# Performance work log

Measured on AMD Instinct MI355X. Metric: run time of the kernel, lower is better.

Reference implementation:

```python
import jax, jax.numpy as jnp
import numpy as np

N_USERS = 10000
N_ITEMS = 40000
HID = 64
NNZ = 2_000_000
B = 8192
N_TOT = N_USERS + N_ITEMS
HOP = 3


def setup_inputs() -> dict:
    key = jax.random.key(0)
    ks = jax.random.split(key, 13)
    emb = lambda k, n: jax.random.normal(k, (n, HID), dtype=jnp.float32) * (1.0 / np.sqrt(HID))
    # Dense social adjacency; scaled so repeated propagation stays numerically stable
    S = jax.random.uniform(ks[6], (N_USERS, N_USERS), dtype=jnp.float32) * (2.0 / N_USERS)
    return {
        "users": jax.random.randint(ks[0], (B,), 0, N_USERS),
        "pos": jax.random.randint(ks[1], (B,), 0, N_ITEMS),
        "neg": jax.random.randint(ks[2], (B,), 0, N_ITEMS),
        "user_embs": emb(ks[3], N_USERS),
        "item_embs": emb(ks[4], N_ITEMS),
        "user1_embs": emb(ks[5], N_USERS),
        "item1_embs": emb(ks[7], N_ITEMS),
        "user2_embs": emb(ks[8], N_USERS),
        "item2_embs": emb(ks[9], N_ITEMS),
        "S": S,
        "A_rows": jax.random.randint(ks[10], (NNZ,), 0, N_TOT, dtype=jnp.int32),
        "A_cols": jax.random.randint(ks[11], (NNZ,), 0, N_TOT, dtype=jnp.int32),
        "A_vals": jax.random.uniform(ks[12], (NNZ,), dtype=jnp.float32) * (1.0 / 40.0),
        "hop": HOP,
    }


def social_gcn(uemb, S, hop):
    # LightGCN-style propagation over dense social graph; mean over layers 0..hop
    h = uemb
    acc = uemb
    for _ in range(hop):
        h = S @ h                      # [n_users, hid] dense GEMM
        acc = acc + h
    return acc / (hop + 1)


def ui_gcn(uemb, iemb, rows, cols, vals, hop):
    # LightGCN over sparse bipartite user-item graph of size [N_TOT, N_TOT]
    ego = jnp.concatenate([uemb, iemb], axis=0)   # [N_TOT, hid]
    h = ego
    acc = ego
    for _ in range(hop):
        msgs = vals[:, None] * h[cols]            # gather + scale  [nnz, hid]
        h = jax.ops.segment_sum(msgs, rows, num_segments=N_TOT)
        acc = acc + h
    out = acc / (hop + 1)
    return out[:N_USERS], out[N_USERS:]


def reference(users, pos, neg, user_embs, item_embs, user1_embs, item1_embs,
              user2_embs, item2_embs, S, A_rows, A_cols, A_vals, hop):
    all_user_S = social_gcn(user_embs, S, hop)
    all_user_A, all_item = ui_gcn(user_embs, item_embs, A_rows, A_cols, A_vals, hop)
    all_user = 0.5 * all_user_S + 0.5 * all_user_A

    all_user_social = social_gcn(user1_embs, S, hop)
    all_item_social = item1_embs
    all_user_rating, all_item_rating = ui_gcn(user2_embs, item2_embs, A_rows, A_cols, A_vals, hop)

    return (all_user[users], all_item[pos], all_item[neg],
            all_user_S, all_user_A,
            all_user_social[users], all_item_social[pos], all_item_social[neg],
            all_user_rating[users], all_item_rating[pos], all_item_rating[neg])
```

## Files before the change

kernel.cpp:

```cpp
#include <hip/hip_runtime.h>

#define N_USERS 10000
#define N_ITEMS 40000
#define N_TOTAL 50000
#define HID     64
#define BATCH   8192
#define HOPS    3
#define KDIM    10000
#define KTILES  157
#define KPAD    (KTILES * 64)
#define SPLITK  4
#define NSOC    (KTILES * SPLITK)

#define O0 0
#define O1 524288
#define O2 1048576
#define O3 1572864
#define O4 2212864
#define O5 2852864
#define O6 3377152
#define O7 3901440
#define O8 4425728
#define O9 4950016
#define O10 5474304

typedef __attribute__((ext_vector_type(8))) short short8;
typedef __attribute__((ext_vector_type(4))) float floatx4;
typedef __attribute__((ext_vector_type(4))) unsigned short ushort4v;
typedef __attribute__((ext_vector_type(8))) unsigned short ushort8v;

__device__ __forceinline__ unsigned short f32bf(float f) {
  union { float f; unsigned u; } v; v.f = f;
  unsigned r = v.u + 0x7fffu + ((v.u >> 16) & 1u);
  return (unsigned short)(r >> 16);
}

__global__ __launch_bounds__(256)
void init_all(const float* __restrict__ ue, const float* __restrict__ u1,
              const float* __restrict__ ie, const float* __restrict__ u2,
              const float* __restrict__ i2, const int* __restrict__ Arows,
              int* __restrict__ counts, int nnz,
              float* __restrict__ HS0, float* __restrict__ HS1, float* __restrict__ HSacc,
              float* __restrict__ E0, float* __restrict__ Eacc) {
  int b = blockIdx.x, t = threadIdx.x;
  if (b < 2500) {
    int i = b * 256 + t;
    int r = i >> 6, c = i & 63;
    float a = ue[i], x = u1[i];
    size_t p = (size_t)r * 128 + c;
    HS0[p] = a; HS0[p + 64] = x;
    HSacc[p] = a; HSacc[p + 64] = x;
    HS1[p] = 0.f; HS1[p + 64] = 0.f;
  } else if (b < 15000) {
    int i = (b - 2500) * 256 + t;
    int r = i >> 6;
    float a, x;
    if (r < N_USERS) { a = ue[i]; x = u2[i]; }
    else             { a = ie[i - N_USERS * HID]; x = i2[i - N_USERS * HID]; }
    size_t p = (size_t)r * 128 + (i & 63);
    E0[p] = a; E0[p + 64] = x;
    Eacc[p] = a; Eacc[p + 64] = x;
  } else {
    int i = (b - 15000) * 256 + t;
    if (i < nnz) atomicAdd(&counts[Arows[i]], 1);
  }
}

__global__ void scan1(const int* __restrict__ counts, int* __restrict__ offs, int* __restrict__ bsum) {
  __shared__ int sh[256];
  int t = threadIdx.x;
  int base = blockIdx.x * 1024 + t * 4;
  int v0 = 0, v1 = 0, v2 = 0, v3 = 0;
  if (base + 0 < N_TOTAL) v0 = counts[base + 0];
  if (base + 1 < N_TOTAL) v1 = counts[base + 1];
  if (base + 2 < N_TOTAL) v2 = counts[base + 2];
  if (base + 3 < N_TOTAL) v3 = counts[base + 3];
  int s = v0 + v1 + v2 + v3;
  sh[t] = s;
  __syncthreads();
  for (int d = 1; d < 256; d <<= 1) {
    int x = (t >= d) ? sh[t - d] : 0;
    __syncthreads();
    sh[t] += x;
    __syncthreads();
  }
  int excl = sh[t] - s;
  if (t == 255) bsum[blockIdx.x] = sh[255];
  if (base + 0 < N_TOTAL) offs[base + 0] = excl; excl += v0;
  if (base + 1 < N_TOTAL) offs[base + 1] = excl; excl += v1;
  if (base + 2 < N_TOTAL) offs[base + 2] = excl; excl += v2;
  if (base + 3 < N_TOTAL) offs[base + 3] = excl;
}

__global__ void scan2(int* __restrict__ bsum, int nb) {
  __shared__ int sh[64];
  int t = threadIdx.x;
  int v = (t < nb) ? bsum[t] : 0;
  sh[t] = v;
  __syncthreads();
  for (int d = 1; d < 64; d <<= 1) {
    int x = (t >= d) ? sh[t - d] : 0;
    __syncthreads();
    sh[t] += x;
    __syncthreads();
  }
  if (t < nb) bsum[t] = sh[t] - v;
}

__device__ __forceinline__ void transpose_dev(int kb, const float* __restrict__ H,
                                              unsigned short* __restrict__ Ht,
                                              float* __restrict__ ts) {
  int k0 = kb * 64;
  int t = threadIdx.x;
#pragma unroll
  for (int i = 0; i < 8; i++) {
    int f = t + i * 256;
    int r = f >> 5, c4 = (f & 31) * 4;
    float4 v = make_float4(0.f, 0.f, 0.f, 0.f);
    if (k0 + r < KDIM) v = *(const float4*)&H[(size_t)(k0 + r) * 128 + c4];
    *(float4*)&ts[r * 132 + c4] = v;
  }
  __syncthreads();
#pragma unroll
  for (int i = 0; i < 4; i++) {
    int g = t + i * 256;
    int n = g >> 3, ko = (g & 7) * 8;
    ushort8v o;
#pragma unroll
    for (int j = 0; j < 8; j++) o[j] = f32bf(ts[(ko + j) * 132 + n]);
    *(ushort8v*)&Ht[(size_t)n * KPAD + k0 + ko] = o;
  }
}

__global__ __launch_bounds__(256)
void scan3_tr(int* __restrict__ offs, const int* __restrict__ bexcl,
              int* __restrict__ cursor, int nnz,
              const float* __restrict__ hc, unsigned short* __restrict__ Ht) {
  __shared__ __align__(16) float ts[64 * 132];
  if (blockIdx.x < 196) {
    int i = blockIdx.x * 256 + threadIdx.x;
    if (i < N_TOTAL) {
      int v = offs[i] + bexcl[i >> 10];
      offs[i] = v; cursor[i] = v;
    }
    if (i == 0) offs[N_TOTAL] = nnz;
  } else {
    transpose_dev(blockIdx.x - 196, hc, Ht, ts);
  }
}

__global__ void scatter_csr(const int* __restrict__ rows, const int* __restrict__ cols,
                            const float* __restrict__ vals, int* __restrict__ cursor,
                            int2* __restrict__ edges, int n) {
  int i = blockIdx.x * 256 + threadIdx.x;
  if (i < n) {
    int p = atomicAdd(&cursor[rows[i]], 1);
    edges[p] = make_int2(cols[i], __float_as_int(vals[i]));
  }
}

template<int H>
__global__ __launch_bounds__(256)
void social_gemm(const float* __restrict__ S, unsigned short* __restrict__ Sb,
                 const unsigned short* __restrict__ Bt, float* __restrict__ Cdst) {
  __shared__ __align__(16) unsigned short As[64 * 72];
  __shared__ __align__(16) unsigned short Bs[128 * 72];
  int tid = threadIdx.x;
  int mt = blockIdx.x % KTILES;
  int ks = blockIdx.x / KTILES;
  int m0 = mt * 64;
  int t0 = (ks * KTILES) / SPLITK;
  int t1 = ((ks + 1) * KTILES) / SPLITK;
  int wave = tid >> 6, lane = tid & 63;
  int mq = lane & 15, quad = lane >> 4;

  floatx4 acc[8];
#pragma unroll
  for (int i = 0; i < 8; i++) acc[i] = (floatx4){0.f, 0.f, 0.f, 0.f};

  int ar = tid >> 2;
  int aq = tid & 3;
  bool rok = (m0 + ar) < KDIM;
  const float* arow = S + (size_t)(m0 + ar) * KDIM;
  unsigned short* sbrow = Sb + (size_t)(m0 + ar) * KPAD;
  int bn = tid >> 3;
  int bk = (tid & 7) * 8;

  for (int t = t0; t < t1; ++t) {
    int k0 = t * 64;
    int kk0 = k0 + aq * 16;
    ushort8v x0 = {0, 0, 0, 0, 0, 0, 0, 0}, x1 = {0, 0, 0, 0, 0, 0, 0, 0};
    if (H == 0) {
      if (rok) {
        if (kk0 < KDIM) {
          floatx4 v0 = __builtin_nontemporal_load((const floatx4*)(arow + kk0));
          floatx4 v1 = __builtin_nontemporal_load((const floatx4*)(arow + kk0 + 4));
          floatx4 v2 = __builtin_nontemporal_load((const floatx4*)(arow + kk0 + 8));
          floatx4 v3 = __builtin_nontemporal_load((const floatx4*)(arow + kk0 + 12));
          x0[0] = f32bf(v0[0]); x0[1] = f32bf(v0[1]); x0[2] = f32bf(v0[2]); x0[3] = f32bf(v0[3]);
          x0[4] = f32bf(v1[0]); x0[5] = f32bf(v1[1]); x0[6] = f32bf(v1[2]); x0[7] = f32bf(v1[3]);
          x1[0] = f32bf(v2[0]); x1[1] = f32bf(v2[1]); x1[2] = f32bf(v2[2]); x1[3] = f32bf(v2[3]);
          x1[4] = f32bf(v3[0]); x1[5] = f32bf(v3[1]); x1[6] = f32bf(v3[2]); x1[7] = f32bf(v3[3]);
        }
        *(ushort8v*)&sbrow[kk0] = x0;
        *(ushort8v*)&sbrow[kk0 + 8] = x1;
      }
    } else {
      if (rok) {
        x0 = *(const ushort8v*)&sbrow[kk0];
        x1 = *(const ushort8v*)&sbrow[kk0 + 8];
      }
    }
    *(ushort8v*)&As[ar * 72 + aq * 16] = x0;
    *(ushort8v*)&As[ar * 72 + aq * 16 + 8] = x1;
#pragma unroll
    for (int i = 0; i < 4; i++) {
      int n = bn + i * 32;
      *(ushort8v*)&Bs[n * 72 + bk] = *(const ushort8v*)&Bt[(size_t)n * KPAD + k0 + bk];
    }
    __syncthreads();
#pragma unroll
    for (int kk = 0; kk < 64; kk += 32) {
      short8 a = *(const short8*)&As[(wave * 16 + mq) * 72 + kk + quad * 8];
#pragma unroll
      for (int nt = 0; nt < 8; nt++) {
        short8 b = *(const short8*)&Bs[(nt * 16 + mq) * 72 + kk + quad * 8];
        acc[nt] = __builtin_amdgcn_mfma_f32_16x16x32_bf16(a, b, acc[nt], 0, 0, 0);
      }
    }
    __syncthreads();
  }
#pragma unroll
  for (int nt = 0; nt < 8; nt++) {
    int col = nt * 16 + mq;
    int rbase = m0 + wave * 16 + quad * 4;
#pragma unroll
    for (int i = 0; i < 4; i++) {
      int r = rbase + i;
      if (r < KDIM) atomicAdd(&Cdst[(size_t)r * 128 + col], acc[nt][i]);
    }
  }
}

template<int LAST>
__global__ __launch_bounds__(256)
void ui_hop(const int* __restrict__ offs, const int2* __restrict__ edges,
            const float* __restrict__ Ein, float* __restrict__ Eout,
            float* __restrict__ Eacc) {
  int wid = blockIdx.x * 4 + (threadIdx.x >> 6);
  int lane2 = (threadIdx.x & 63) * 2;
  const float* Einl = Ein + lane2;
  int s = offs[wid], e = offs[wid + 1];
  float ax = 0.f, ay = 0.f;
  int j = s;
  for (; j + 4 <= e; j += 4) {
    int2 e0 = edges[j], e1 = edges[j + 1], e2 = edges[j + 2], e3 = edges[j + 3];
    float2 p0 = *(const float2*)&Einl[(size_t)e0.x * 128];
    float2 p1 = *(const float2*)&Einl[(size_t)e1.x * 128];
    float2 p2 = *(const float2*)&Einl[(size_t)e2.x * 128];
    float2 p3 = *(const float2*)&Einl[(size_t)e3.x * 128];
    float w0 = __int_as_float(e0.y), w1 = __int_as_float(e1.y);
    float w2 = __int_as_float(e2.y), w3 = __int_as_float(e3.y);
    ax += w0 * p0.x + w1 * p1.x + w2 * p2.x + w3 * p3.x;
    ay += w0 * p0.y + w1 * p1.y + w2 * p2.y + w3 * p3.y;
  }
  for (; j < e; ++j) {
    int2 ed = edges[j];
    float2 p = *(const float2*)&Einl[(size_t)ed.x * 128];
    float w = __int_as_float(ed.y);
    ax += w * p.x; ay += w * p.y;
  }
  size_t op = (size_t)wid * 128 + lane2;
  if (!LAST) { float2 o; o.x = ax; o.y = ay; *(float2*)&Eout[op] = o; }
  float2 a = *(float2*)&Eacc[op];
  a.x += ax; a.y += ay;
  *(float2*)&Eacc[op] = a;
}

template<int H>
__global__ __launch_bounds__(256)
void prep_kernel(const float* __restrict__ hc, unsigned short* __restrict__ Ht,
                 float* __restrict__ HSacc, float* __restrict__ hn) {
  __shared__ __align__(16) float ts[64 * 132];
  if (blockIdx.x < KTILES) {
    transpose_dev(blockIdx.x, hc, Ht, ts);
  } else {
    int i = (blockIdx.x - KTILES) * 256 + threadIdx.x;
    if (i < (N_USERS * 128) / 4) {
      float4 h = ((const float4*)hc)[i];
      float4 a = ((float4*)HSacc)[i];
      a.x += h.x; a.y += h.y; a.z += h.z; a.w += h.w;
      ((float4*)HSacc)[i] = a;
      if (H == 1) ((float4*)hn)[i] = make_float4(0.f, 0.f, 0.f, 0.f);
    }
  }
}

__global__ __launch_bounds__(256)
void out_kernel(const int* __restrict__ users, const int* __restrict__ pos,
                const int* __restrict__ neg, const float* __restrict__ HSacc,
                const float* __restrict__ Eacc, const float* __restrict__ item1,
                float* __restrict__ out) {
  if (blockIdx.x < 2500) {
    int i = blockIdx.x * 256 + threadIdx.x;
    int r = i >> 6, c = i & 63;
    out[O3 + i] = HSacc[(size_t)r * 128 + c] * 0.25f;
    out[O4 + i] = Eacc[(size_t)r * 128 + c] * 0.25f;
  } else {
    int b = (blockIdx.x - 2500) * 4 + (threadIdx.x >> 6);
    int lane = threadIdx.x & 63;
    int u = users[b], p = pos[b], n = neg[b];
    const float q = 0.25f;
    float us = HSacc[(size_t)u * 128 + lane] * q;
    float ua = Eacc[(size_t)u * 128 + lane] * q;
    size_t bl = (size_t)b * 64 + lane;
    out[O0 + bl]  = 0.5f * (us + ua);
    out[O1 + bl]  = Eacc[(size_t)(N_USERS + p) * 128 + lane] * q;
    out[O2 + bl]  = Eacc[(size_t)(N_USERS + n) * 128 + lane] * q;
    out[O5 + bl]  = HSacc[(size_t)u * 128 + 64 + lane] * q;
    out[O6 + bl]  = item1[(size_t)p * 64 + lane];
    out[O7 + bl]  = item1[(size_t)n * 64 + lane];
    out[O8 + bl]  = Eacc[(size_t)u * 128 + 64 + lane] * q;
    out[O9 + bl]  = Eacc[(size_t)(N_USERS + p) * 128 + 64 + lane] * q;
    out[O10 + bl] = Eacc[(size_t)(N_USERS + n) * 128 + 64 + lane] * q;
  }
}

extern "C" void kernel_launch(void* const* d_in, const int* in_sizes, int n_in,
                              void* d_out, int out_size, void* d_ws, size_t ws_size,
                              hipStream_t stream) {
  (void)n_in; (void)out_size; (void)ws_size;
  const int*   users = (const int*)d_in[0];
  const int*   pos   = (const int*)d_in[1];
  const int*   neg   = (const int*)d_in[2];
  const float* ue    = (const float*)d_in[3];
  const float* ie    = (const float*)d_in[4];
  const float* u1    = (const float*)d_in[5];
  const float* i1    = (const float*)d_in[6];
  const float* u2    = (const float*)d_in[7];
  const float* i2    = (const float*)d_in[8];
  const float* S     = (const float*)d_in[9];
  const int*   Arows = (const int*)d_in[10];
  const int*   Acols = (const int*)d_in[11];
  const float* Avals = (const float*)d_in[12];
  const int nnz = in_sizes[10];

  char* ws = (char*)d_ws;
  size_t off = 0;
  auto alloc = [&](size_t b) { size_t r = off; off += (b + 255) & ~(size_t)255; return r; };
  float* HS0   = (float*)(ws + alloc(sizeof(float) * (size_t)N_USERS * 128));
  float* HS1   = (float*)(ws + alloc(sizeof(float) * (size_t)N_USERS * 128));
  float* HSacc = (float*)(ws + alloc(sizeof(float) * (size_t)N_USERS * 128));
  unsigned short* Ht = (unsigned short*)(ws + alloc(sizeof(short) * (size_t)128 * KPAD));
  unsigned short* Sb = (unsigned short*)(ws + alloc(sizeof(short) * (size_t)KDIM * KPAD));
  float* E0    = (float*)(ws + alloc(sizeof(float) * (size_t)N_TOTAL * 128));
  float* E1    = (float*)(ws + alloc(sizeof(float) * (size_t)N_TOTAL * 128));
  float* Eacc  = (float*)(ws + alloc(sizeof(float) * (size_t)N_TOTAL * 128));
  int* counts  = (int*)(ws + alloc(sizeof(int) * (N_TOTAL + 16)));
  int* offs    = (int*)(ws + alloc(sizeof(int) * (N_TOTAL + 16)));
  int* cursor  = (int*)(ws + alloc(sizeof(int) * (N_TOTAL + 16)));
  int* bsum    = (int*)(ws + alloc(sizeof(int) * 256));
  int2* edges  = (int2*)(ws + alloc(sizeof(int2) * (size_t)nnz));

  const int histB = (nnz + 255) / 256;

  hipMemsetAsync(counts, 0, sizeof(int) * (N_TOTAL + 16), stream);
  init_all<<<15000 + histB, 256, 0, stream>>>(ue, u1, ie, u2, i2, Arows, counts, nnz,
                                              HS0, HS1, HSacc, E0, Eacc);
  scan1<<<49, 256, 0, stream>>>(counts, offs, bsum);
  scan2<<<1, 64, 0, stream>>>(bsum, 49);
  scan3_tr<<<196 + KTILES, 256, 0, stream>>>(offs, bsum, cursor, nnz, HS0, Ht);
  scatter_csr<<<histB, 256, 0, stream>>>(Arows, Acols, Avals, cursor, edges, nnz);

  ui_hop<0><<<12500, 256, 0, stream>>>(offs, edges, E0, E1, Eacc);
  social_gemm<0><<<NSOC, 256, 0, stream>>>(S, Sb, Ht, HS1);
  prep_kernel<1><<<KTILES + 1250, 256, 0, stream>>>(HS1, Ht, HSacc, HS0);
  ui_hop<0><<<12500, 256, 0, stream>>>(offs, edges, E1, E0, Eacc);
  social_gemm<1><<<NSOC, 256, 0, stream>>>(S, Sb, Ht, HS0);
  prep_kernel<2><<<KTILES + 1250, 256, 0, stream>>>(HS0, Ht, HSacc, HS1);
  ui_hop<1><<<12500, 256, 0, stream>>>(offs, edges, E0, E1, Eacc);
  social_gemm<2><<<NSOC, 256, 0, stream>>>(S, Sb, Ht, HSacc);

  float* out = (float*)d_out;
  out_kernel<<<2500 + 2048, 256, 0, stream>>>(users, pos, neg, HSacc, Eacc, i1, out);
}
```

Baseline: 1.614 ms.

## Pre-swizzle GEMM operands into MFMA fragment layout and drop LDS staging

The social GEMM now stores the bf16 copy of S and the transposed hidden matrix directly in MFMA register-fragment order, so each lane loads its operands with contiguous 16-byte global reads and no shared memory or barriers. The M tile grows to 128 rows with two row fragments per wave, and split-K rises from 4 to 8 to keep the grid large. The cost is no LDS reuse of B across waves, since each wave reads the B fragments from global/L2 itself.

Result: faster. 1.521 ms (-5.8%).

```diff
diff --git a/kernel.cpp b/kernel.cpp
--- a/kernel.cpp
+++ b/kernel.cpp
@@ -9,8 +9,9 @@
 #define KDIM    10000
 #define KTILES  157
 #define KPAD    (KTILES * 64)
-#define SPLITK  4
-#define NSOC    (KTILES * SPLITK)
+#define MTILES  79
+#define SPLITK  8
+#define NSOC    (MTILES * SPLITK)
 
 #define O0 0
 #define O1 524288
@@ -26,13 +27,20 @@
 
 typedef __attribute__((ext_vector_type(8))) short short8;
 typedef __attribute__((ext_vector_type(4))) float floatx4;
-typedef __attribute__((ext_vector_type(4))) unsigned short ushort4v;
-typedef __attribute__((ext_vector_type(8))) unsigned short ushort8v;
 
 __device__ __forceinline__ unsigned short f32bf(float f) {
   union { float f; unsigned u; } v; v.f = f;
   unsigned r = v.u + 0x7fffu + ((v.u >> 16) & 1u);
   return (unsigned short)(r >> 16);
+}
+
+__device__ __forceinline__ short8 cvt8(floatx4 v0, floatx4 v1) {
+  short8 o;
+  o[0] = (short)f32bf(v0[0]); o[1] = (short)f32bf(v0[1]);
+  o[2] = (short)f32bf(v0[2]); o[3] = (short)f32bf(v0[3]);
+  o[4] = (short)f32bf(v1[0]); o[5] = (short)f32bf(v1[1]);
+  o[6] = (short)f32bf(v1[2]); o[7] = (short)f32bf(v1[3]);
+  return o;
 }
 
 __global__ __launch_bounds__(256)
@@ -107,14 +115,14 @@
   if (t < nb) bsum[t] = sh[t] - v;
 }
 
-__device__ __forceinline__ void transpose_dev(int kb, const float* __restrict__ H,
-                                              unsigned short* __restrict__ Ht,
-                                              float* __restrict__ ts) {
-  int k0 = kb * 64;
-  int t = threadIdx.x;
+__device__ __forceinline__ void bfrag_dev(int t, const float* __restrict__ H,
+                                          unsigned short* __restrict__ Bf,
+                                          float* __restrict__ ts) {
+  int k0 = t * 64;
+  int tid = threadIdx.x;
 #pragma unroll
   for (int i = 0; i < 8; i++) {
-    int f = t + i * 256;
+    int f = tid + i * 256;
     int r = f >> 5, c4 = (f & 31) * 4;
     float4 v = make_float4(0.f, 0.f, 0.f, 0.f);
     if (k0 + r < KDIM) v = *(const float4*)&H[(size_t)(k0 + r) * 128 + c4];
@@ -123,19 +131,21 @@
   __syncthreads();
 #pragma unroll
   for (int i = 0; i < 4; i++) {
-    int g = t + i * 256;
-    int n = g >> 3, ko = (g & 7) * 8;
-    ushort8v o;
-#pragma unroll
-    for (int j = 0; j < 8; j++) o[j] = f32bf(ts[(ko + j) * 132 + n]);
-    *(ushort8v*)&Ht[(size_t)n * KPAD + k0 + ko] = o;
-  }
-}
-
-__global__ __launch_bounds__(256)
-void scan3_tr(int* __restrict__ offs, const int* __restrict__ bexcl,
+    int c0 = tid + i * 256;
+    int nt = c0 >> 7, kk = (c0 >> 6) & 1, l = c0 & 63;
+    int quad = l >> 4, mq = l & 15;
+    short8 o;
+#pragma unroll
+    for (int j = 0; j < 8; j++)
+      o[j] = (short)f32bf(ts[(kk * 32 + quad * 8 + j) * 132 + nt * 16 + mq]);
+    *(short8*)&Bf[(((size_t)t * 8 + nt) * 2 + kk) * 512 + l * 8] = o;
+  }
+}
+
+__global__ __launch_bounds__(256)
+void scan3_bf(int* __restrict__ offs, const int* __restrict__ bexcl,
               int* __restrict__ cursor, int nnz,
-              const float* __restrict__ hc, unsigned short* __restrict__ Ht) {
+              const float* __restrict__ hc, unsigned short* __restrict__ Bf) {
   __shared__ __align__(16) float ts[64 * 132];
   if (blockIdx.x < 196) {
     int i = blockIdx.x * 256 + threadIdx.x;
@@ -145,7 +155,7 @@
     }
     if (i == 0) offs[N_TOTAL] = nnz;
   } else {
-    transpose_dev(blockIdx.x - 196, hc, Ht, ts);
+    bfrag_dev(blockIdx.x - 196, hc, Bf, ts);
   }
 }
 
@@ -161,83 +171,90 @@
 
 template<int H>
 __global__ __launch_bounds__(256)
-void social_gemm(const float* __restrict__ S, unsigned short* __restrict__ Sb,
-                 const unsigned short* __restrict__ Bt, float* __restrict__ Cdst) {
-  __shared__ __align__(16) unsigned short As[64 * 72];
-  __shared__ __align__(16) unsigned short Bs[128 * 72];
+void social_gemm(const float* __restrict__ S, unsigned short* __restrict__ Sbf,
+                 const unsigned short* __restrict__ Bf, float* __restrict__ Cdst) {
   int tid = threadIdx.x;
-  int mt = blockIdx.x % KTILES;
-  int ks = blockIdx.x / KTILES;
-  int m0 = mt * 64;
+  int w = tid >> 6, lane = tid & 63;
+  int quad = lane >> 4, mq = lane & 15;
+  int mtile = blockIdx.x % MTILES;
+  int ks = blockIdx.x / MTILES;
+  int m0 = mtile * 128;
   int t0 = (ks * KTILES) / SPLITK;
   int t1 = ((ks + 1) * KTILES) / SPLITK;
-  int wave = tid >> 6, lane = tid & 63;
-  int mq = lane & 15, quad = lane >> 4;
-
-  floatx4 acc[8];
-#pragma unroll
-  for (int i = 0; i < 8; i++) acc[i] = (floatx4){0.f, 0.f, 0.f, 0.f};
-
-  int ar = tid >> 2;
-  int aq = tid & 3;
-  bool rok = (m0 + ar) < KDIM;
-  const float* arow = S + (size_t)(m0 + ar) * KDIM;
-  unsigned short* sbrow = Sb + (size_t)(m0 + ar) * KPAD;
-  int bn = tid >> 3;
-  int bk = (tid & 7) * 8;
+
+  floatx4 acc[2][8];
+#pragma unroll
+  for (int rf = 0; rf < 2; rf++)
+#pragma unroll
+    for (int nt = 0; nt < 8; nt++) acc[rf][nt] = (floatx4){0.f, 0.f, 0.f, 0.f};
+
+  int r0 = m0 + w * 32 + mq;
+  int r1 = r0 + 16;
+  const float* sr0 = S + (size_t)r0 * KDIM;
+  const float* sr1 = S + (size_t)r1 * KDIM;
+  size_t sb = (((size_t)mtile * KTILES) * 8 + w * 2) * 1024 + (size_t)lane * 8;
 
   for (int t = t0; t < t1; ++t) {
-    int k0 = t * 64;
-    int kk0 = k0 + aq * 16;
-    ushort8v x0 = {0, 0, 0, 0, 0, 0, 0, 0}, x1 = {0, 0, 0, 0, 0, 0, 0, 0};
+    short8 a00, a01, a10, a11;
+    size_t st = sb + (size_t)t * 8192;
     if (H == 0) {
-      if (rok) {
-        if (kk0 < KDIM) {
-          floatx4 v0 = __builtin_nontemporal_load((const floatx4*)(arow + kk0));
-          floatx4 v1 = __builtin_nontemporal_load((const floatx4*)(arow + kk0 + 4));
-          floatx4 v2 = __builtin_nontemporal_load((const floatx4*)(arow + kk0 + 8));
-          floatx4 v3 = __builtin_nontemporal_load((const floatx4*)(arow + kk0 + 12));
-          x0[0] = f32bf(v0[0]); x0[1] = f32bf(v0[1]); x0[2] = f32bf(v0[2]); x0[3] = f32bf(v0[3]);
-          x0[4] = f32bf(v1[0]); x0[5] = f32bf(v1[1]); x0[6] = f32bf(v1[2]); x0[7] = f32bf(v1[3]);
-          x1[0] = f32bf(v2[0]); x1[1] = f32bf(v2[1]); x1[2] = f32bf(v2[2]); x1[3] = f32bf(v2[3]);
-          x1[4] = f32bf(v3[0]); x1[5] = f32bf(v3[1]); x1[6] = f32bf(v3[2]); x1[7] = f32bf(v3[3]);
-        }
-        *(ushort8v*)&sbrow[kk0] = x0;
-        *(ushort8v*)&sbrow[kk0 + 8] = x1;
+      int kb = t * 64 + quad * 8;
+      a00 = a01 = a10 = a11 = (short8){0, 0, 0, 0, 0, 0, 0, 0};
+      {
+        int k = kb;
+        if (r0 < KDIM && k < KDIM)
+          a00 = cvt8(__builtin_nontemporal_load((const floatx4*)(sr0 + k)),
+                     __builtin_nontemporal_load((const floatx4*)(sr0 + k + 4)));
+        k = kb + 32;
+        if (r0 < KDIM && k < KDIM)
+          a01 = cvt8(__builtin_nontemporal_load((const floatx4*)(sr0 + k)),
+                     __builtin_nontemporal_load((const floatx4*)(sr0 + k + 4)));
+        k = kb;
+        if (r1 < KDIM && k < KDIM)
+          a10 = cvt8(__builtin_nontemporal_load((const floatx4*)(sr1 + k)),
+                     __builtin_nontemporal_load((const floatx4*)(sr1 + k + 4)));
+        k = kb + 32;
+        if (r1 < KDIM && k < KDIM)
+          a11 = cvt8(__builtin_nontemporal_load((const floatx4*)(sr1 + k)),
+                     __builtin_nontemporal_load((const floatx4*)(sr1 + k + 4)));
       }
+      *(short8*)&Sbf[st]        = a00;
+      *(short8*)&Sbf[st + 512]  = a01;
+      *(short8*)&Sbf[st + 1024] = a10;
+      *(short8*)&Sbf[st + 1536] = a11;
     } else {
-      if (rok) {
-        x0 = *(const ushort8v*)&sbrow[kk0];
-        x1 = *(const ushort8v*)&sbrow[kk0 + 8];
+      a00 = *(const short8*)&Sbf[st];
+      a01 = *(const short8*)&Sbf[st + 512];
+      a10 = *(const short8*)&Sbf[st + 1024];
+      a11 = *(const short8*)&Sbf[st + 1536];
+    }
+    const unsigned short* bfb = Bf + (size_t)t * 8192 + lane * 8;
+#pragma unroll
+    for (int kk = 0; kk < 2; kk++) {
+      short8 b[8];
+#pragma unroll
+      for (int nt = 0; nt < 8; nt++)
+        b[nt] = *(const short8*)&bfb[((size_t)nt * 2 + kk) * 512];
+      short8 ax0 = kk ? a01 : a00;
+      short8 ax1 = kk ? a11 : a10;
+#pragma unroll
+      for (int nt = 0; nt < 8; nt++) {
+        acc[0][nt] = __builtin_amdgcn_mfma_f32_16x16x32_bf16(ax0, b[nt], acc[0][nt], 0, 0, 0);
+        acc[1][nt] = __builtin_amdgcn_mfma_f32_16x16x32_bf16(ax1, b[nt], acc[1][nt], 0, 0, 0);
       }
     }
-    *(ushort8v*)&As[ar * 72 + aq * 16] = x0;
-    *(ushort8v*)&As[ar * 72 + aq * 16 + 8] = x1;
-#pragma unroll
-    for (int i = 0; i < 4; i++) {
-      int n = bn + i * 32;
-      *(ushort8v*)&Bs[n * 72 + bk] = *(const ushort8v*)&Bt[(size_t)n * KPAD + k0 + bk];
-    }
-    __syncthreads();
-#pragma unroll
-    for (int kk = 0; kk < 64; kk += 32) {
-      short8 a = *(const short8*)&As[(wave * 16 + mq) * 72 + kk + quad * 8];
-#pragma unroll
-      for (int nt = 0; nt < 8; nt++) {
-        short8 b = *(const short8*)&Bs[(nt * 16 + mq) * 72 + kk + quad * 8];
-        acc[nt] = __builtin_amdgcn_mfma_f32_16x16x32_bf16(a, b, acc[nt], 0, 0, 0);
+  }
+#pragma unroll
+  for (int rf = 0; rf < 2; rf++) {
+    int rb = m0 + w * 32 + rf * 16 + quad * 4;
+#pragma unroll
+    for (int nt = 0; nt < 8; nt++) {
+      int col = nt * 16 + mq;
+#pragma unroll
+      for (int i = 0; i < 4; i++) {
+        int r = rb + i;
+        if (r < KDIM) atomicAdd(&Cdst[(size_t)r * 128 + col], acc[rf][nt][i]);
       }
-    }
-    __syncthreads();
-  }
-#pragma unroll
-  for (int nt = 0; nt < 8; nt++) {
-    int col = nt * 16 + mq;
-    int rbase = m0 + wave * 16 + quad * 4;
-#pragma unroll
-    for (int i = 0; i < 4; i++) {
-      int r = rbase + i;
-      if (r < KDIM) atomicAdd(&Cdst[(size_t)r * 128 + col], acc[nt][i]);
     }
   }
 }
@@ -279,11 +296,11 @@
 
 template<int H>
 __global__ __launch_bounds__(256)
-void prep_kernel(const float* __restrict__ hc, unsigned short* __restrict__ Ht,
+void prep_kernel(const float* __restrict__ hc, unsigned short* __restrict__ Bf,
                  float* __restrict__ HSacc, float* __restrict__ hn) {
   __shared__ __align__(16) float ts[64 * 132];
   if (blockIdx.x < KTILES) {
-    transpose_dev(blockIdx.x, hc, Ht, ts);
+    bfrag_dev(blockIdx.x, hc, Bf, ts);
   } else {
     int i = (blockIdx.x - KTILES) * 256 + threadIdx.x;
     if (i < (N_USERS * 128) / 4) {
@@ -351,8 +368,8 @@
   float* HS0   = (float*)(ws + alloc(sizeof(float) * (size_t)N_USERS * 128));
   float* HS1   = (float*)(ws + alloc(sizeof(float) * (size_t)N_USERS * 128));
   float* HSacc = (float*)(ws + alloc(sizeof(float) * (size_t)N_USERS * 128));
-  unsigned short* Ht = (unsigned short*)(ws + alloc(sizeof(short) * (size_t)128 * KPAD));
-  unsigned short* Sb = (unsigned short*)(ws + alloc(sizeof(short) * (size_t)KDIM * KPAD));
+  unsigned short* Bf  = (unsigned short*)(ws + alloc(sizeof(short) * (size_t)KTILES * 8192));
+  unsigned short* Sbf = (unsigned short*)(ws + alloc(sizeof(short) * (size_t)MTILES * KTILES * 8192));
   float* E0    = (float*)(ws + alloc(sizeof(float) * (size_t)N_TOTAL * 128));
   float* E1    = (float*)(ws + alloc(sizeof(float) * (size_t)N_TOTAL * 128));
   float* Eacc  = (float*)(ws + alloc(sizeof(float) * (size_t)N_TOTAL * 128));
@@ -369,17 +386,17 @@
                                               HS0, HS1, HSacc, E0, Eacc);
   scan1<<<49, 256, 0, stream>>>(counts, offs, bsum);
   scan2<<<1, 64, 0, stream>>>(bsum, 49);
-  scan3_tr<<<196 + KTILES, 256, 0, stream>>>(offs, bsum, cursor, nnz, HS0, Ht);
+  scan3_bf<<<196 + KTILES, 256, 0, stream>>>(offs, bsum, cursor, nnz, HS0, Bf);
   scatter_csr<<<histB, 256, 0, stream>>>(Arows, Acols, Avals, cursor, edges, nnz);
 
   ui_hop<0><<<12500, 256, 0, stream>>>(offs, edges, E0, E1, Eacc);
-  social_gemm<0><<<NSOC, 256, 0, stream>>>(S, Sb, Ht, HS1);
-  prep_kernel<1><<<KTILES + 1250, 256, 0, stream>>>(HS1, Ht, HSacc, HS0);
+  social_gemm<0><<<NSOC, 256, 0, stream>>>(S, Sbf, Bf, HS1);
+  prep_kernel<1><<<KTILES + 1250, 256, 0, stream>>>(HS1, Bf, HSacc, HS0);
   ui_hop<0><<<12500, 256, 0, stream>>>(offs, edges, E1, E0, Eacc);
-  social_gemm<1><<<NSOC, 256, 0, stream>>>(S, Sb, Ht, HS0);
-  prep_kernel<2><<<KTILES + 1250, 256, 0, stream>>>(HS0, Ht, HSacc, HS1);
+  social_gemm<1><<<NSOC, 256, 0, stream>>>(S, Sbf, Bf, HS0);
+  prep_kernel<2><<<KTILES + 1250, 256, 0, stream>>>(HS0, Bf, HSacc, HS1);
   ui_hop<1><<<12500, 256, 0, stream>>>(offs, edges, E0, E1, Eacc);
-  social_gemm<2><<<NSOC, 256, 0, stream>>>(S, Sb, Ht, HSacc);
+  social_gemm<2><<<NSOC, 256, 0, stream>>>(S, Sbf, Bf, HSacc);
 
   float* out = (float*)d_out;
   out_kernel<<<2500 + 2048, 256, 0, stream>>>(users, pos, neg, HSacc, Eacc, i1, out);
```
